# Kernel tuning notes

Hardware: AMD Instinct MI355X
Metric: run time of the kernel (lower is better)

Reference implementation:

```python
import jax, jax.numpy as jnp
import numpy as np

NUM_HEADS = 12   # H
NUM_TASKS = 4    # T
TOP_K = 2        # capacity_factor


def setup_inputs() -> dict:
    key = jax.random.key(0)
    ks = jax.random.split(key, 4)
    B, N, C = 2, 4100, 768  # N = NUM_TASKS + M, M = 4096
    x = jax.random.normal(ks[0], (B, N, C), dtype=jnp.float32)
    # torch.nn.Linear weights are [out_features, in_features]; y = x @ W.T
    qs_w = jax.random.normal(ks[1], (NUM_TASKS, C, C), dtype=jnp.float32) * 0.02
    kv_w = jax.random.normal(ks[2], (2 * C, C), dtype=jnp.float32) * 0.02
    experts_w = jax.random.normal(ks[3], (NUM_TASKS, C, C), dtype=jnp.float32) * 0.02
    return {"x": x, "qs_w": qs_w, "kv_w": kv_w, "experts_w": experts_w}


def reference(x, qs_w, kv_w, experts_w):
    B, N, C = x.shape
    T, H, K = NUM_TASKS, NUM_HEADS, TOP_K
    d = C // H
    M = N - T
    scale = d ** -0.5

    feature = x[:, T:, :]                                    # [B,M,C]
    kv = (feature @ kv_w.T).reshape(B, M, 2, H, d)
    k = jnp.transpose(kv[:, :, 0], (0, 2, 1, 3))             # [B,H,M,d]
    v = jnp.transpose(kv[:, :, 1], (0, 2, 1, 3))             # [B,H,M,d]

    # per-task q projections on task tokens (qs_w[t] is [out,in])
    q = jnp.einsum('btc,toc->bto', x[:, :T], qs_w)           # [B,T,C]
    q = q.reshape(B, T, H, d).transpose(0, 2, 1, 3)          # [B,H,T,d]

    attn = jnp.einsum('bhtd,bhmd->bhtm', q, k) * scale       # [B,H,T,M]
    topv, topi = jax.lax.top_k(attn, K)                      # [B,H,T,K]
    topw = jax.nn.softmax(topv, axis=-1)                     # softmax over top-k only

    # scatter softmaxed top-k back into dense [B,H,T,M] (indices unique per row)
    oh = jax.nn.one_hot(topi, M, dtype=x.dtype)              # [B,H,T,K,M]
    attn_topk = jnp.einsum('bhtk,bhtkm->bhtm', topw, oh)
    attn_token = jnp.einsum('bhtm,bhmd->bhtd', attn_topk, v)
    attn_token = attn_token.transpose(0, 2, 1, 3).reshape(B, T, C)   # [B,T,C]

    # gather top-k feature rows per head/task, weight, and scatter back
    fm = feature.reshape(B, M, H, d).transpose(0, 2, 1, 3)   # [B,H,M,d]
    feat_topk = jnp.take_along_axis(fm[:, :, None], topi[..., None], axis=3)  # [B,H,T,K,d]
    feat_topk = feat_topk * topw[..., None]
    # scatter to [B,H,T,M,d], then permute(0,2,3,1,4)+reshape -> [B,T,M,C]
    feat_pad = jnp.einsum('bhtkd,bhtkm->btmhd', feat_topk, oh).reshape(B, T, M, C)

    # per-task experts (no bias); einsum('btnc,btnc->bnc') with ones = sum over t
    feature_output = jnp.einsum('btmc,toc->bmo', feat_pad, experts_w)  # [B,M,C]
    token_output = jnp.einsum('btc,toc->bto', attn_token, experts_w)   # [B,T,C]

    return jnp.concatenate([token_output, feature_output], axis=1)     # [B,N,C]
```

## Files before the change

kernel.cpp:

```cpp
#include <hip/hip_runtime.h>
#include <math.h>

#define B_ 2
#define N_ 4100
#define C_ 768
#define T_ 4
#define H_ 12
#define D_ 64
#define M_ 4096
#define S_ 48
#define KS_ 12
#define KC_ 64
#define NJ_ 16
#define MT_ 128
#define SEG_ 8
#define GRID_ 768
#define SCALE 0.125f

__device__ __forceinline__ bool better(float va, int ia, float vb, int ib) {
  return (va > vb) || (va == vb && ia < ib);
}

__device__ __forceinline__ void merge2(float& v1, int& i1, float& v2, int& i2,
                                       float ov1, int oi1, float ov2, int oi2) {
  if (better(ov1, oi1, v1, i1)) {
    float tv; int ti;
    tv = v1; ti = i1; v1 = ov1; i1 = oi1; ov1 = tv; oi1 = ti;
    tv = v2; ti = i2; v2 = ov2; i2 = oi2; ov2 = tv; oi2 = ti;
  }
  if (better(ov1, oi1, v2, i2)) { v2 = ov1; i2 = oi1; }
}

__global__ __launch_bounds__(256) void qkzero_kernel(const float* __restrict__ x,
    const float* __restrict__ qs_w, const float* __restrict__ kv_w,
    float* __restrict__ qk, float* __restrict__ out) {
  const int blk = blockIdx.x;
  const int tid = threadIdx.x;
  if (blk < B_ * S_) {
    const int h = blk % H_;
    const int t = (blk / H_) % T_;
    const int b = blk / S_;
    __shared__ float xs[C_];
    __shared__ float red[256];
    __shared__ float qseg[D_];
    for (int i = tid; i < C_; i += 256) xs[i] = x[((size_t)b * N_ + t) * C_ + i];
    __syncthreads();
    {
      const int j = tid & 63;
      const int pt = tid >> 6;
      const float* wr = qs_w + ((size_t)t * C_ + h * D_ + j) * C_ + pt * 192;
      float a = 0.f;
      for (int c = 0; c < 192; ++c) a += xs[pt * 192 + c] * wr[c];
      red[tid] = a;
    }
    __syncthreads();
    if (tid < 64)
      qseg[tid] = (red[tid] + red[tid + 64] + red[tid + 128] + red[tid + 192]) * SCALE;
    __syncthreads();
    for (int c = tid; c < C_; c += 256) {
      float a = 0.f;
      #pragma unroll 8
      for (int j = 0; j < 64; ++j) a += qseg[j] * kv_w[((size_t)(h * D_ + j)) * C_ + c];
      qk[(size_t)blk * C_ + c] = a;
    }
  } else {
    const int zb = blk - B_ * S_;
    const int NV4 = (B_ * N_ * C_) / 4;
    float4 z = make_float4(0.f, 0.f, 0.f, 0.f);
    float4* ov = (float4*)out;
    for (int i = zb * 256 + tid; i < NV4; i += (GRID_ - B_ * S_) * 256) ov[i] = z;
  }
}

__global__ __launch_bounds__(256, 3) void score_kernel(const float* __restrict__ x,
    const float* __restrict__ qk, float* __restrict__ part) {
  const int bm = blockIdx.x & 31;
  const int b  = blockIdx.x >> 5;
  const int kc = blockIdx.y;
  const int tid = threadIdx.x;

  __shared__ __align__(16) float fbuf[MT_][68];
  __shared__ __align__(16) float qbuf[S_][KC_];

  {
    const char* xb = (const char*)(x + ((size_t)b * N_ + T_ + bm * MT_) * C_ + kc * KC_);
    #pragma unroll
    for (int i = 0; i < 8; ++i) {
      unsigned g = i * 256 + tid;
      unsigned r = g >> 4, j = g & 15;
      *(float4*)&fbuf[r][j * 4] = *(const float4*)(xb + (size_t)r * (C_ * 4) + j * 16);
    }
  }
  {
    const char* qb = (const char*)(qk + (size_t)b * S_ * C_ + kc * KC_);
    #pragma unroll
    for (int i = 0; i < 3; ++i) {
      unsigned g = i * 256 + tid;
      unsigned s = g >> 4, j = g & 15;
      *(float4*)&qbuf[s][j * 4] = *(const float4*)(qb + (size_t)s * (C_ * 4) + j * 16);
    }
  }
  __syncthreads();

  const int w = tid >> 6;
  const int lane = tid & 63;
  const int s0 = w * 12;

  float acc[12][2];
  #pragma unroll
  for (int si = 0; si < 12; ++si) {
    acc[si][0] = 0.f; acc[si][1] = 0.f;
  }

  #pragma unroll 2
  for (int j = 0; j < NJ_; ++j) {
    float4 f0 = *(const float4*)&fbuf[lane     ][j * 4];
    float4 f1 = *(const float4*)&fbuf[lane + 64][j * 4];
    #pragma unroll
    for (int si = 0; si < 12; ++si) {
      float4 q = *(const float4*)&qbuf[s0 + si][j * 4];
      acc[si][0] += f0.x * q.x + f0.y * q.y + f0.z * q.z + f0.w * q.w;
      acc[si][1] += f1.x * q.x + f1.y * q.y + f1.z * q.z + f1.w * q.w;
    }
  }

  const int m0 = bm * MT_;
  #pragma unroll
  for (int si = 0; si < 12; ++si) {
    float* pp = part + (((size_t)kc * B_ + b) * S_ + (s0 + si)) * M_ + m0 + lane;
    pp[0]  = acc[si][0];
    pp[64] = acc[si][1];
  }
}

__global__ __launch_bounds__(256) void reduce_kernel(const float* __restrict__ part,
                                                     float* __restrict__ cand) {
  const int seg = blockIdx.x & 7;
  const int bs = blockIdx.x >> 3;
  const int tid = threadIdx.x;
  const size_t kstride = (size_t)B_ * S_ * M_;
  const float* p0 = part + (size_t)bs * M_ + seg * 512 + tid * 2;
  float a0 = 0.f, a1 = 0.f;
  #pragma unroll
  for (int kc = 0; kc < KS_; ++kc) {
    float2 v = *(const float2*)(p0 + kc * kstride);
    a0 += v.x; a1 += v.y;
  }
  const int mA = seg * 512 + tid * 2;
  float v1, v2; int i1, i2;
  if (better(a0, mA, a1, mA + 1)) { v1 = a0; i1 = mA; v2 = a1; i2 = mA + 1; }
  else                            { v1 = a1; i1 = mA + 1; v2 = a0; i2 = mA; }
  #pragma unroll
  for (int off = 1; off < 64; off <<= 1) {
    float ov1 = __shfl_xor(v1, off);
    int   oi1 = __shfl_xor(i1, off);
    float ov2 = __shfl_xor(v2, off);
    int   oi2 = __shfl_xor(i2, off);
    merge2(v1, i1, v2, i2, ov1, oi1, ov2, oi2);
  }
  __shared__ float cbuf[4][4];
  const int w = tid >> 6, lane = tid & 63;
  if (lane == 0) {
    cbuf[w][0] = v1; ((int*)cbuf[w])[1] = i1;
    cbuf[w][2] = v2; ((int*)cbuf[w])[3] = i2;
  }
  __syncthreads();
  if (tid == 0) {
    for (int ww = 1; ww < 4; ++ww)
      merge2(v1, i1, v2, i2, cbuf[ww][0], ((int*)cbuf[ww])[1],
             cbuf[ww][2], ((int*)cbuf[ww])[3]);
    ((float4*)cand)[blockIdx.x] =
        make_float4(v1, __int_as_float(i1), v2, __int_as_float(i2));
  }
}

__global__ __launch_bounds__(256) void gather_kernel(const float* __restrict__ x,
    const float* __restrict__ kv_w, const float* __restrict__ experts_w,
    const float* __restrict__ cand, float* __restrict__ out) {
  const int h = blockIdx.x % H_;
  const int t = (blockIdx.x / H_) % T_;
  const int b = blockIdx.x / S_;
  const int tid = threadIdx.x;

  __shared__ __align__(16) float f0[C_], f1[C_], fc[C_];
  __shared__ float red[256];
  __shared__ __align__(16) float attnh[D_];
  __shared__ float sel[4];

  if (tid < 8) {
    float4 cv = ((const float4*)cand)[blockIdx.x * 8 + tid];
    float v1 = cv.x, v2 = cv.z;
    int i1 = __float_as_int(cv.y), i2 = __float_as_int(cv.w);
    #pragma unroll
    for (int off = 1; off < 8; off <<= 1) {
      float ov1 = __shfl_xor(v1, off);
      int   oi1 = __shfl_xor(i1, off);
      float ov2 = __shfl_xor(v2, off);
      int   oi2 = __shfl_xor(i2, off);
      merge2(v1, i1, v2, i2, ov1, oi1, ov2, oi2);
    }
    if (tid == 0) {
      float w1 = 1.f / (1.f + expf(v2 - v1));
      ((int*)sel)[0] = i1; ((int*)sel)[1] = i2;
      sel[2] = w1; sel[3] = 1.f - w1;
    }
  }
  __syncthreads();
  const int i1 = ((const int*)sel)[0];
  const int i2 = ((const int*)sel)[1];
  const float w1 = sel[2], w2 = sel[3];

  const float* r0 = x + ((size_t)b * N_ + T_ + i1) * C_;
  const float* r1 = x + ((size_t)b * N_ + T_ + i2) * C_;
  for (int i = tid; i < C_; i += 256) {
    float a = r0[i], bb = r1[i];
    f0[i] = a; f1[i] = bb; fc[i] = w1 * a + w2 * bb;
  }
  __syncthreads();

  const int j = tid & 63, pt = tid >> 6;
  {
    const float4* kr4 = (const float4*)(kv_w + ((size_t)(C_ + h * D_ + j)) * C_ + pt * 192);
    const float4* fc4 = (const float4*)(&fc[pt * 192]);
    float a = 0.f;
    #pragma unroll 8
    for (int c4 = 0; c4 < 48; ++c4) {
      float4 kv = kr4[c4], fv = fc4[c4];
      a += kv.x * fv.x + kv.y * fv.y + kv.z * fv.z + kv.w * fv.w;
    }
    red[tid] = a;
  }
  __syncthreads();
  if (tid < 64)
    attnh[tid] = red[tid] + red[tid + 64] + red[tid + 128] + red[tid + 192];
  __syncthreads();

  const size_t ot = ((size_t)b * N_ + t) * C_;
  const size_t o0 = ((size_t)b * N_ + T_ + i1) * C_;
  const size_t o1 = ((size_t)b * N_ + T_ + i2) * C_;
  for (int o = tid; o < C_; o += 256) {
    const float4* er4 = (const float4*)(experts_w + ((size_t)t * C_ + o) * C_ + h * D_);
    const float4* at4 = (const float4*)attnh;
    const float4* g04 = (const float4*)&f0[h * D_];
    const float4* g14 = (const float4*)&f1[h * D_];
    float at = 0.f, a0 = 0.f, a1 = 0.f;
    #pragma unroll
    for (int c4 = 0; c4 < 16; ++c4) {
      float4 e = er4[c4];
      float4 av = at4[c4], v0 = g04[c4], v1 = g14[c4];
      at += e.x * av.x + e.y * av.y + e.z * av.z + e.w * av.w;
      a0 += e.x * v0.x + e.y * v0.y + e.z * v0.z + e.w * v0.w;
      a1 += e.x * v1.x + e.y * v1.y + e.z * v1.z + e.w * v1.w;
    }
    atomicAdd(&out[ot + o], at);
    atomicAdd(&out[o0 + o], w1 * a0);
    atomicAdd(&out[o1 + o], w2 * a1);
  }
}

extern "C" void kernel_launch(void* const* d_in, const int* in_sizes, int n_in,
                              void* d_out, int out_size, void* d_ws, size_t ws_size,
                              hipStream_t stream) {
  const float* x         = (const float*)d_in[0];
  const float* qs_w      = (const float*)d_in[1];
  const float* kv_w      = (const float*)d_in[2];
  const float* experts_w = (const float*)d_in[3];
  float* out = (float*)d_out;

  float* ws   = (float*)d_ws;
  float* qk   = ws;
  float* part = qk + (size_t)B_ * S_ * C_;
  float* cand = part + (size_t)KS_ * B_ * S_ * M_;

  hipLaunchKernelGGL(qkzero_kernel, dim3(GRID_),          dim3(256), 0, stream, x, qs_w, kv_w, qk, out);
  hipLaunchKernelGGL(score_kernel,  dim3(B_ * 32, KS_),   dim3(256), 0, stream, x, qk, part);
  hipLaunchKernelGGL(reduce_kernel, dim3(B_ * S_ * SEG_), dim3(256), 0, stream, part, cand);
  hipLaunchKernelGGL(gather_kernel, dim3(B_ * S_),        dim3(256), 0, stream, x, kv_w, experts_w, cand, out);
}
```

Baseline: 140.2 us.

## Split gather kernel into value projection and parallel expert scatter kernels

```diff
diff --git a/kernel.cpp b/kernel.cpp
--- a/kernel.cpp
+++ b/kernel.cpp
@@ -174,17 +174,15 @@
   }
 }
 
-__global__ __launch_bounds__(256) void gather_kernel(const float* __restrict__ x,
-    const float* __restrict__ kv_w, const float* __restrict__ experts_w,
-    const float* __restrict__ cand, float* __restrict__ out) {
+__global__ __launch_bounds__(256) void gatherA_kernel(const float* __restrict__ x,
+    const float* __restrict__ kv_w, const float* __restrict__ cand,
+    float* __restrict__ selws) {
   const int h = blockIdx.x % H_;
-  const int t = (blockIdx.x / H_) % T_;
   const int b = blockIdx.x / S_;
   const int tid = threadIdx.x;
 
-  __shared__ __align__(16) float f0[C_], f1[C_], fc[C_];
+  __shared__ __align__(16) float fc[C_];
   __shared__ float red[256];
-  __shared__ __align__(16) float attnh[D_];
   __shared__ float sel[4];
 
   if (tid < 8) {
@@ -212,14 +210,12 @@
 
   const float* r0 = x + ((size_t)b * N_ + T_ + i1) * C_;
   const float* r1 = x + ((size_t)b * N_ + T_ + i2) * C_;
-  for (int i = tid; i < C_; i += 256) {
-    float a = r0[i], bb = r1[i];
-    f0[i] = a; f1[i] = bb; fc[i] = w1 * a + w2 * bb;
-  }
-  __syncthreads();
-
-  const int j = tid & 63, pt = tid >> 6;
+  for (int i = tid; i < C_; i += 256)
+    fc[i] = w1 * r0[i] + w2 * r1[i];
+  __syncthreads();
+
   {
+    const int j = tid & 63, pt = tid >> 6;
     const float4* kr4 = (const float4*)(kv_w + ((size_t)(C_ + h * D_ + j)) * C_ + pt * 192);
     const float4* fc4 = (const float4*)(&fc[pt * 192]);
     float a = 0.f;
@@ -232,17 +228,43 @@
   }
   __syncthreads();
   if (tid < 64)
-    attnh[tid] = red[tid] + red[tid + 64] + red[tid + 128] + red[tid + 192];
-  __syncthreads();
-
-  const size_t ot = ((size_t)b * N_ + t) * C_;
-  const size_t o0 = ((size_t)b * N_ + T_ + i1) * C_;
-  const size_t o1 = ((size_t)b * N_ + T_ + i2) * C_;
-  for (int o = tid; o < C_; o += 256) {
+    selws[(size_t)blockIdx.x * 72 + tid] =
+        red[tid] + red[tid + 64] + red[tid + 128] + red[tid + 192];
+  else if (tid < 68)
+    selws[(size_t)blockIdx.x * 72 + tid] = sel[tid - 64];
+}
+
+__global__ __launch_bounds__(256) void scatter_kernel(const float* __restrict__ x,
+    const float* __restrict__ experts_w, const float* __restrict__ selws,
+    float* __restrict__ out) {
+  const int bs = blockIdx.x >> 3, oc = blockIdx.x & 7;
+  const int h = bs % H_;
+  const int t = (bs / H_) % T_;
+  const int b = bs / S_;
+  const int tid = threadIdx.x;
+
+  __shared__ __align__(16) float attnh[D_], g0s[D_], g1s[D_];
+  __shared__ float psel[4];
+
+  if (tid < 4) psel[tid] = selws[(size_t)bs * 72 + 64 + tid];
+  __syncthreads();
+  const int i1 = __float_as_int(psel[0]);
+  const int i2 = __float_as_int(psel[1]);
+  const float w1 = psel[2], w2 = psel[3];
+
+  if (tid < 64) {
+    attnh[tid] = selws[(size_t)bs * 72 + tid];
+    g0s[tid] = x[((size_t)b * N_ + T_ + i1) * C_ + h * D_ + tid];
+    g1s[tid] = x[((size_t)b * N_ + T_ + i2) * C_ + h * D_ + tid];
+  }
+  __syncthreads();
+
+  if (tid < 96) {
+    const int o = oc * 96 + tid;
     const float4* er4 = (const float4*)(experts_w + ((size_t)t * C_ + o) * C_ + h * D_);
     const float4* at4 = (const float4*)attnh;
-    const float4* g04 = (const float4*)&f0[h * D_];
-    const float4* g14 = (const float4*)&f1[h * D_];
+    const float4* g04 = (const float4*)g0s;
+    const float4* g14 = (const float4*)g1s;
     float at = 0.f, a0 = 0.f, a1 = 0.f;
     #pragma unroll
     for (int c4 = 0; c4 < 16; ++c4) {
@@ -252,9 +274,9 @@
       a0 += e.x * v0.x + e.y * v0.y + e.z * v0.z + e.w * v0.w;
       a1 += e.x * v1.x + e.y * v1.y + e.z * v1.z + e.w * v1.w;
     }
-    atomicAdd(&out[ot + o], at);
-    atomicAdd(&out[o0 + o], w1 * a0);
-    atomicAdd(&out[o1 + o], w2 * a1);
+    atomicAdd(&out[((size_t)b * N_ + t) * C_ + o], at);
+    atomicAdd(&out[((size_t)b * N_ + T_ + i1) * C_ + o], w1 * a0);
+    atomicAdd(&out[((size_t)b * N_ + T_ + i2) * C_ + o], w2 * a1);
   }
 }
 
@@ -267,13 +289,15 @@
   const float* experts_w = (const float*)d_in[3];
   float* out = (float*)d_out;
 
-  float* ws   = (float*)d_ws;
-  float* qk   = ws;
-  float* part = qk + (size_t)B_ * S_ * C_;
-  float* cand = part + (size_t)KS_ * B_ * S_ * M_;
-
-  hipLaunchKernelGGL(qkzero_kernel, dim3(GRID_),          dim3(256), 0, stream, x, qs_w, kv_w, qk, out);
-  hipLaunchKernelGGL(score_kernel,  dim3(B_ * 32, KS_),   dim3(256), 0, stream, x, qk, part);
-  hipLaunchKernelGGL(reduce_kernel, dim3(B_ * S_ * SEG_), dim3(256), 0, stream, part, cand);
-  hipLaunchKernelGGL(gather_kernel, dim3(B_ * S_),        dim3(256), 0, stream, x, kv_w, experts_w, cand, out);
-}
+  float* ws    = (float*)d_ws;
+  float* qk    = ws;
+  float* part  = qk + (size_t)B_ * S_ * C_;
+  float* cand  = part + (size_t)KS_ * B_ * S_ * M_;
+  float* selws = cand + (size_t)B_ * S_ * SEG_ * 4;
+
+  hipLaunchKernelGGL(qkzero_kernel,  dim3(GRID_),          dim3(256), 0, stream, x, qs_w, kv_w, qk, out);
+  hipLaunchKernelGGL(score_kernel,   dim3(B_ * 32, KS_),   dim3(256), 0, stream, x, qk, part);
+  hipLaunchKernelGGL(reduce_kernel,  dim3(B_ * S_ * SEG_), dim3(256), 0, stream, part, cand);
+  hipLaunchKernelGGL(gatherA_kernel, dim3(B_ * S_),        dim3(256), 0, stream, x, kv_w, cand, selws);
+  hipLaunchKernelGGL(scatter_kernel, dim3(B_ * S_ * 8),    dim3(256), 0, stream, x, experts_w, selws, out);
+}
```

Result: no change. 139.8 us (-0.3%).
